# Performance work log

Measured on AMD Instinct MI355X. Metric: run time of the kernel, lower is better.

The kernel has to match this reference:

```python
import jax, jax.numpy as jnp
import numpy as np

B, T, E, A, S, H = 1024, 64, 1024, 10, 30, 200  # batch, time, embed, actdim, stoch, deter==hidden
MIN_STD = 0.1


def _xavier(key, fan_in, fan_out):
    lim = float(np.sqrt(6.0 / (fan_in + fan_out)))
    return jax.random.uniform(key, (fan_in, fan_out), jnp.float32, -lim, lim)


def setup_inputs() -> dict:
    key = jax.random.key(0)
    ks = jax.random.split(key, 20)
    gl = 1.0 / float(np.sqrt(H))  # torch GRUCell default init bound
    inp = {
        'embed': jax.random.normal(ks[0], (B, T, E), jnp.float32),
        'action': jax.random.normal(ks[1], (B, T, A), jnp.float32),
        'eps_post': jax.random.normal(ks[2], (T, B, S), jnp.float32),
        'eps_prior': jax.random.normal(ks[3], (T, B, S), jnp.float32),
        # Linear weights stored [in, out] (transposed vs torch) so x @ W works.
        'img1_w': _xavier(ks[4], A + S, H), 'img1_b': jnp.zeros((H,), jnp.float32),
        'gru_wi': jax.random.uniform(ks[5], (H, 3 * H), jnp.float32, -gl, gl),
        'gru_wh': jax.random.uniform(ks[6], (H, 3 * H), jnp.float32, -gl, gl),
        'gru_bi': jax.random.uniform(ks[7], (3 * H,), jnp.float32, -gl, gl),
        'gru_bh': jax.random.uniform(ks[8], (3 * H,), jnp.float32, -gl, gl),
        'img2_w': _xavier(ks[9], H, H), 'img2_b': jnp.zeros((H,), jnp.float32),
        'img3_w': _xavier(ks[10], H, 2 * S), 'img3_b': jnp.zeros((2 * S,), jnp.float32),
        'obs1_w': _xavier(ks[11], H + E, H), 'obs1_b': jnp.zeros((H,), jnp.float32),
        'obs2_w': _xavier(ks[12], H, 2 * S), 'obs2_b': jnp.zeros((2 * S,), jnp.float32),
    }
    return inp


def _observe(embed, action, eps_post, eps_prior,
             img1_w, img1_b, gru_wi, gru_wh, gru_bi, gru_bh,
             img2_w, img2_b, img3_w, img3_b, obs1_w, obs1_b, obs2_w, obs2_b):
    elu = jax.nn.elu
    embed_t = jnp.transpose(embed, (1, 0, 2))   # [T,B,E]
    action_t = jnp.transpose(action, (1, 0, 2))  # [T,B,A]

    def step(carry, xs):
        stoch, deter = carry
        a, emb, ep_q, ep_p = xs
        # img_step (prior)
        x = elu(jnp.concatenate([stoch, a], -1) @ img1_w + img1_b)
        gi = x @ gru_wi + gru_bi
        gh = deter @ gru_wh + gru_bh
        ir, iz, i_n = jnp.split(gi, 3, axis=-1)
        hr, hz, h_n = jnp.split(gh, 3, axis=-1)
        r = jax.nn.sigmoid(ir + hr)
        z = jax.nn.sigmoid(iz + hz)
        n = jnp.tanh(i_n + r * h_n)
        deter = (1.0 - z) * n + z * deter
        y = elu(deter @ img2_w + img2_b) @ img3_w + img3_b
        p_mean, p_std = jnp.split(y, 2, axis=-1)
        p_std = jax.nn.softplus(p_std) + MIN_STD
        p_stoch = p_mean + p_std * ep_p  # rsample
        # obs_step (posterior)
        o = elu(jnp.concatenate([deter, emb], -1) @ obs1_w + obs1_b) @ obs2_w + obs2_b
        q_mean, q_std = jnp.split(o, 2, axis=-1)
        q_std = jax.nn.softplus(q_std) + MIN_STD
        q_stoch = q_mean + q_std * ep_q  # rsample
        out = jnp.concatenate([q_mean, q_std, q_stoch, deter,
                               p_mean, p_std, p_stoch, deter], axis=-1)
        return (q_stoch, deter), out

    init = (jnp.zeros((B, S), embed.dtype), jnp.zeros((B, H), embed.dtype))
    _, outs = jax.lax.scan(step, init, (action_t, embed_t, eps_post, eps_prior))
    # outs: [T, B, 2*(3S+H)] -> [B, T, 580]; layout: post(mean,std,stoch,deter)|prior(mean,std,stoch,deter)
    return jnp.transpose(outs, (1, 0, 2))


def reference(embed, action, eps_post, eps_prior,
              img1_w, img1_b, gru_wi, gru_wh, gru_bi, gru_bh,
              img2_w, img2_b, img3_w, img3_b, obs1_w, obs1_b, obs2_w, obs2_b):
    return _observe(embed, action, eps_post, eps_prior,
                    img1_w, img1_b, gru_wi, gru_wh, gru_bi, gru_bh,
                    img2_w, img2_b, img3_w, img3_b, obs1_w, obs1_b, obs2_w, obs2_b)
```

## Files before the change

kernel.cpp:

```cpp
#include <hip/hip_runtime.h>

#define T_ 64

typedef __attribute__((ext_vector_type(4))) float f32x4;
typedef __attribute__((ext_vector_type(8))) short s16x8;

__device__ __forceinline__ unsigned short f2bf(float f) {
  unsigned u = __float_as_uint(f);
  u = (u + 0x7FFFu + ((u >> 16) & 1u)) >> 16;
  return (unsigned short)u;
}
__device__ __forceinline__ float bf2f(unsigned short h) {
  return __uint_as_float(((unsigned)h) << 16);
}
__device__ __forceinline__ float eluf(float x) { return x > 0.f ? x : __expf(x) - 1.f; }
__device__ __forceinline__ float sigmf(float x) { return 1.f / (1.f + __expf(-x)); }
__device__ __forceinline__ float tanh_(float x) {
  float xx = fminf(fmaxf(x, -30.f), 30.f);
  float e = __expf(-2.f * xx);
  return (1.f - e) / (1.f + e);
}
__device__ __forceinline__ float softpf(float x) {
  return x > 20.f ? x : __logf(1.f + __expf(x));
}

#define OPW1   0
#define OPWI   6656
#define OPWH   126464
#define OPO1D  246272
#define OPO2   286208
#define OPI2   298496
#define OPI3   345088
#define OWIWT  359424
#define OWHWT  364416
#define OO1DWT 369408
#define OI1WT  371072
#define OO2WT  372736
#define PK_U16 373248

#define OFF_PK  26214400
#define OFF_SWZ 26960896

__device__ void pack_mat(int idx, int stride, const float* __restrict__ W,
                         int K, int N, int KT, int NT, unsigned short* __restrict__ dst) {
  int total = KT * NT * 512;
  for (int i = idx; i < total; i += stride) {
    int j = i & 7, l = (i >> 3) & 63, rem = i >> 9;
    int kt = rem % KT, nt = rem / KT;
    int n = nt * 16 + (l & 15), k = kt * 32 + (l >> 4) * 8 + j;
    float v = (k < K && n < N) ? W[(size_t)k * N + n] : 0.f;
    dst[i] = f2bf(v);
  }
}

__device__ void pack_gate(int idx, int stride, const float* __restrict__ W,
                          unsigned short* __restrict__ dst) {
  int total = 3 * 13 * 6 * 512;
  for (int i = idx; i < total; i += stride) {
    int j = i & 7, l = (i >> 3) & 63, rem = i >> 9;
    int kt = rem % 6, rem2 = rem / 6, nt = rem2 % 13, g = rem2 / 13;
    int u = nt * 16 + (l & 15);
    int k = kt * 32 + (l >> 4) * 8 + j;
    float v = (u < 200) ? W[(size_t)k * 600 + g * 200 + u] : 0.f;
    dst[i] = f2bf(v);
  }
}

__global__ void prep_weights(const float* __restrict__ w1, const float* __restrict__ wi,
                             const float* __restrict__ wh, const float* __restrict__ i2,
                             const float* __restrict__ i3, const float* __restrict__ obs1w,
                             const float* __restrict__ o2,
                             unsigned short* __restrict__ pk,
                             unsigned short* __restrict__ swz) {
  int idx = blockIdx.x * blockDim.x + threadIdx.x;
  int stride = gridDim.x * blockDim.x;
  pack_mat(idx, stride, w1, 40, 200, 1, 13, pk + OPW1);
  pack_gate(idx, stride, wi, pk + OPWI);
  pack_gate(idx, stride, wh, pk + OPWH);
  pack_mat(idx, stride, obs1w, 200, 200, 6, 13, pk + OPO1D);
  pack_mat(idx, stride, o2, 200, 60, 6, 4, pk + OPO2);
  pack_mat(idx, stride, i2, 200, 200, 7, 13, pk + OPI2);
  pack_mat(idx, stride, i3, 200, 60, 7, 4, pk + OPI3);
  for (int i = idx; i < 4992; i += stride) {
    int j = i & 7, c = (i >> 3) % 208, g = i / 1664;
    pk[OWIWT + i] = f2bf((c < 200) ? wi[(size_t)(192 + j) * 600 + g * 200 + c] : 0.f);
    pk[OWHWT + i] = f2bf((c < 200) ? wh[(size_t)(192 + j) * 600 + g * 200 + c] : 0.f);
  }
  for (int i = idx; i < 1664; i += stride) {
    int c = i >> 3, j = i & 7;
    pk[OO1DWT + i] = f2bf((c < 200) ? obs1w[(size_t)(192 + j) * 200 + c] : 0.f);
    pk[OI1WT + i]  = f2bf((c < 200) ? w1[(size_t)(32 + j) * 200 + c] : 0.f);
  }
  for (int i = idx; i < 512; i += stride) {
    int c = i >> 3, j = i & 7;
    pk[OO2WT + i] = f2bf((c < 60) ? o2[(size_t)(192 + j) * 60 + c] : 0.f);
  }
  for (int i = idx; i < 212992; i += stride) {
    int j = i & 7, l = (i >> 3) & 63, rem = i >> 9;
    int nt = rem % 13, kc = rem / 13;
    int k = kc * 32 + ((l >> 4) * 8) + j;
    int n = nt * 16 + (l & 15);
    float v = (n < 200) ? obs1w[(size_t)(200 + k) * 200 + n] : 0.0f;
    swz[i] = f2bf(v);
  }
}

__global__ __launch_bounds__(256) void emb_gemm(const float* __restrict__ embed,
                                                const float* __restrict__ obs1b,
                                                const unsigned short* __restrict__ swz,
                                                unsigned short* __restrict__ emb_pre) {
  __shared__ __align__(16) unsigned short lds_A[64][40];
  int tid = threadIdx.x;
  int lane = tid & 63, w = tid >> 6;
  int R0 = blockIdx.x * 64;
  int tt = R0 >> 10;
  int bb = R0 & 1023;

  f32x4 acc[13];
#pragma unroll
  for (int nt = 0; nt < 13; ++nt) acc[nt] = (f32x4){0.f, 0.f, 0.f, 0.f};

  int i_row = tid >> 2, cg = tid & 3;
  const float* arow = embed + ((size_t)(bb + i_row) * 64 + tt) * 1024 + cg * 8;

  for (int kc = 0; kc < 32; ++kc) {
    __syncthreads();
    {
      const float* p = arow + kc * 32;
      f32x4 a0 = *(const f32x4*)p;
      f32x4 a1 = *(const f32x4*)(p + 4);
      unsigned short* dst = &lds_A[i_row][cg * 8];
      dst[0] = f2bf(a0[0]); dst[1] = f2bf(a0[1]); dst[2] = f2bf(a0[2]); dst[3] = f2bf(a0[3]);
      dst[4] = f2bf(a1[0]); dst[5] = f2bf(a1[1]); dst[6] = f2bf(a1[2]); dst[7] = f2bf(a1[3]);
    }
    __syncthreads();
    s16x8 af = *(const s16x8*)&lds_A[w * 16 + (lane & 15)][(lane >> 4) * 8];
    const unsigned short* bp = swz + (size_t)kc * 6656 + (size_t)lane * 8;
#pragma unroll
    for (int nt = 0; nt < 13; ++nt) {
      s16x8 bfv = *(const s16x8*)(bp + nt * 512);
      acc[nt] = __builtin_amdgcn_mfma_f32_16x16x32_bf16(af, bfv, acc[nt], 0, 0, 0);
    }
  }
  int r0 = R0 + w * 16 + ((lane >> 4) << 2);
  int c0 = lane & 15;
#pragma unroll
  for (int nt = 0; nt < 13; ++nt) {
    int n = nt * 16 + c0;
    if (n < 200) {
      float bv = obs1b[n];
#pragma unroll
      for (int rr = 0; rr < 4; ++rr)
        emb_pre[(size_t)(r0 + rr) * 200 + n] = f2bf(acc[nt][rr] + bv);
    }
  }
}

#define LGKM0  asm volatile("s_waitcnt lgkmcnt(0)" ::: "memory")
#define MEMCLB asm volatile("" ::: "memory")
#define BAR()  __builtin_amdgcn_s_barrier()
#define MFMA16(A, B, C) __builtin_amdgcn_mfma_f32_16x16x32_bf16((A), (B), (C), 0, 0, 0)
#define WV9  asm volatile("s_waitcnt vmcnt(9)" ::: "memory")
#define WV29 asm volatile("s_waitcnt vmcnt(29)" ::: "memory")
#define WV4  asm volatile("s_waitcnt vmcnt(4)" ::: "memory")
#define WV0  asm volatile("s_waitcnt vmcnt(0)" ::: "memory")

typedef __attribute__((address_space(3))) unsigned int u32_lds;
typedef const __attribute__((address_space(1))) unsigned int u32_glb;

__device__ __forceinline__ void gll16(const unsigned short* g, unsigned short* l, int lane) {
  __builtin_amdgcn_global_load_lds((u32_glb*)(g + lane * 8), (u32_lds*)l, 16, 0, 0);
}

template <int TB, bool BIGB>
__device__ __forceinline__ f32x4 cons6(const s16x8* A, f32x4 acc,
                                       unsigned short* ringw, const unsigned* toffw,
                                       const unsigned short* pk, int lane) {
#pragma unroll
  for (int kt = 0; kt < 6; ++kt) {
    const int tau = TB + kt;
    if ((tau & 3) == 0) {
      if (tau < 8) { if (BIGB) { WV29; } else { WV9; } }
      else { WV4; }
    }
    s16x8 Bv = *(const s16x8*)(ringw + (tau & 7) * 512 + lane * 8);
    acc = MFMA16(A[kt], Bv, acc);
    if ((tau & 3) == 3) {
      LGKM0; MEMCLB;
#pragma unroll
      for (int k2 = 1; k2 <= 4; ++k2) {
        const int tile = (tau + 4 + k2) % 48;
        gll16(pk + toffw[tile], ringw + (tile & 7) * 512, lane);
      }
      MEMCLB;
    }
  }
  return acc;
}

__device__ __forceinline__ f32x4 res6(const s16x8* A, const s16x8* Wt, f32x4 acc) {
#pragma unroll
  for (int kt = 0; kt < 6; ++kt) acc = MFMA16(A[kt], Wt[kt], acc);
  return acc;
}
__device__ __forceinline__ f32x4 rem1(const s16x8& A6, const unsigned short* wt,
                                      const unsigned short* zb, bool kg0, f32x4 acc) {
  const unsigned short* p = kg0 ? wt : zb;
  return MFMA16(A6, *(const s16x8*)p, acc);
}
__device__ __forceinline__ void grustep(const f32x4& rv, const f32x4& zv,
                                        const f32x4& inv, const f32x4& hnv, f32x4& dv) {
#pragma unroll
  for (int rr = 0; rr < 4; ++rr) {
    float r = sigmf(rv[rr]);
    float z = sigmf(zv[rr]);
    float n = tanh_(inv[rr] + r * hnv[rr]);
    dv[rr] = (1.f - z) * n + z * dv[rr];
  }
}

__global__ __launch_bounds__(512, 1) void scan_v7(
    const float* __restrict__ action, const float* __restrict__ eps_post,
    const float* __restrict__ img1_b, const float* __restrict__ gru_bi,
    const float* __restrict__ gru_bh, const float* __restrict__ obs2_b,
    const unsigned short* __restrict__ pk, const unsigned short* __restrict__ emb_pre,
    float* __restrict__ out) {

  __shared__ __align__(16) unsigned short ring[8][8][512];
  __shared__ __align__(16) unsigned short l_w1[13 * 512];
  __shared__ __align__(16) unsigned short l_wiWT[3][208][8];
  __shared__ __align__(16) unsigned short l_whWT[3][208][8];
  __shared__ __align__(16) unsigned short l_o1dWT[208][8];
  __shared__ __align__(16) unsigned short l_i1WT[208][8];
  __shared__ __align__(16) unsigned short l_o2WT[64][8];
  __shared__ __align__(16) unsigned short zblk[8];
  __shared__ __align__(16) unsigned short xoA[28][16][8];
  __shared__ __align__(16) unsigned short dA[28][16][8];
  __shared__ __align__(16) unsigned short sA[8][16][8];
  __shared__ __align__(16) float s_o[60][20];
  __shared__ __align__(16) float outbuf[16][292];
  __shared__ unsigned l_toff[8][48];

  const int tid = threadIdx.x, lane = tid & 63, w = tid >> 6;
  const int arow = lane & 15, kg = lane >> 4;
  const bool kg0 = (kg == 0);
  const int b0 = blockIdx.x * 16;
  unsigned short* ringw = &ring[w][0][0];
  const unsigned* toffw = &l_toff[w][0];

  for (int i = tid; i < 28 * 16 * 8; i += 512) { (&xoA[0][0][0])[i] = 0; (&dA[0][0][0])[i] = 0; }
  for (int i = tid; i < 8 * 16 * 8; i += 512) (&sA[0][0][0])[i] = 0;
  for (int i = tid; i < 13 * 512; i += 512) l_w1[i] = pk[OPW1 + i];
  for (int i = tid; i < 4992; i += 512) {
    (&l_wiWT[0][0][0])[i] = pk[OWIWT + i];
    (&l_whWT[0][0][0])[i] = pk[OWHWT + i];
  }
  for (int i = tid; i < 1664; i += 512) {
    (&l_o1dWT[0][0])[i] = pk[OO1DWT + i];
    (&l_i1WT[0][0])[i] = pk[OI1WT + i];
  }
  for (int i = tid; i < 512; i += 512) (&l_o2WT[0][0])[i] = pk[OO2WT + i];
  if (tid < 8) zblk[tid] = 0;
  for (int i = tid; i < 8 * 48; i += 512) {
    int ww = i / 48, tau = i % 48;
    unsigned off;
    if (ww < 5) {
      if (tau < 18) { int g = tau / 6, kt = tau % 6; off = OPWI + ((g * 13 + ww) * 6 + kt) * 512; }
      else {
        int t2 = tau - 18, ug = ww + 8;
        if (t2 < 6)       off = OPWI + ((0 * 13 + ug) * 6 + t2) * 512;
        else if (t2 < 12) off = OPWI + ((1 * 13 + ug) * 6 + (t2 - 6)) * 512;
        else if (t2 < 18) off = OPWH + ((1 * 13 + ug) * 6 + (t2 - 12)) * 512;
        else if (t2 < 24) off = OPWI + ((2 * 13 + ug) * 6 + (t2 - 18)) * 512;
        else              off = OPWH + ((2 * 13 + ug) * 6 + (t2 - 24)) * 512;
      }
    } else {
      if (tau < 18) { int g = tau / 6, kt = tau % 6; off = OPWI + ((g * 13 + ww) * 6 + kt) * 512; }
      else if (tau < 42) {
        int i4 = (tau - 18) / 6, kt = (tau - 18) % 6;
        int nt = (ww - 5) * 4 + i4;
        off = OPO1D + (nt * 6 + kt) * 512;
      } else {
        int kt = tau - 42;
        int nt5 = (ww == 5) ? 0 : (ww == 6) ? 1 : 3;
        off = OPO2 + (nt5 * 6 + kt) * 512;
      }
    }
    l_toff[ww][tau] = off;
  }

  s16x8 wB[4][6];
  {
    const unsigned short* base[4];
    if (w < 5) {
      base[0] = pk + OPWH + (size_t)((0 * 13 + w) * 6) * 512;
      base[1] = pk + OPWH + (size_t)((1 * 13 + w) * 6) * 512;
      base[2] = pk + OPWH + (size_t)((2 * 13 + w) * 6) * 512;
      base[3] = pk + OPWH + (size_t)((0 * 13 + w + 8) * 6) * 512;
    } else {
      base[0] = pk + OPWH + (size_t)((0 * 13 + w) * 6) * 512;
      base[1] = pk + OPWH + (size_t)((1 * 13 + w) * 6) * 512;
      base[2] = pk + OPWH + (size_t)((2 * 13 + w) * 6) * 512;
      if (w == 5)      base[3] = pk + OPO1D + (size_t)(12 * 6) * 512;
      else if (w == 7) base[3] = pk + OPO2 + (size_t)(2 * 6) * 512;
      else             base[3] = pk + OPO1D;
    }
#pragma unroll
    for (int s = 0; s < 4; ++s)
#pragma unroll
      for (int kt = 0; kt < 6; ++kt)
        wB[s][kt] = *(const s16x8*)(base[s] + (size_t)kt * 512 + lane * 8);
  }

  const int uA = w * 16 + arow;
  const int uB = (w + 8) * 16 + arow;
  const bool mB = (w < 5) && (uB < 200);
  const int uBc = (uB < 200) ? uB : 199;
  float bsA0 = gru_bi[uA] + gru_bh[uA];
  float bsA1 = gru_bi[200 + uA] + gru_bh[200 + uA];
  float bi2a = gru_bi[400 + uA], bh2a = gru_bh[400 + uA];
  float bsB0 = mB ? (gru_bi[uBc] + gru_bh[uBc]) : 0.f;
  float bsB1 = mB ? (gru_bi[200 + uBc] + gru_bh[200 + uBc]) : 0.f;
  float bi2b = mB ? gru_bi[400 + uBc] : 0.f;
  float bh2b = mB ? gru_bh[400 + uBc] : 0.f;
  float b1A = img1_b[uA];
  float b1B = mB ? img1_b[uBc] : 0.f;
  float b5a = 0.f, b5b = 0.f;
  if (w == 5) b5a = obs2_b[arow];
  else if (w == 6) b5a = obs2_b[16 + arow];
  else if (w == 7) { b5a = (48 + arow < 60) ? obs2_b[48 + arow] : 0.f; b5b = obs2_b[32 + arow]; }

  unsigned short e16[20];
#pragma unroll
  for (int i = 0; i < 20; ++i) e16[i] = 0;
  if (w >= 5) {
#pragma unroll
    for (int i = 0; i < 5; ++i) {
      int nt = (w == 5) ? ((i < 4) ? i : 12) : ((w == 6) ? (4 + ((i < 4) ? i : 3)) : (8 + ((i < 4) ? i : 3)));
      int c = nt * 16 + arow; int cc = (c < 200) ? c : 199;
#pragma unroll
      for (int rr = 0; rr < 4; ++rr)
        e16[i * 4 + rr] = emb_pre[((size_t)(b0 + kg * 4 + rr)) * 200 + cc];
    }
  }
  float epsv;
  { int it = (tid < 480) ? tid : 479;
    epsv = eps_post[((size_t)(b0 + it / 30)) * 30 + it % 30]; }
  float act0, actn;
  { int sl = (lane < 20) ? (w * 20 + lane) : (w * 20);
    act0 = action[((size_t)(b0 + sl / 10) * T_ + 0) * 10 + sl % 10];
    actn = action[((size_t)(b0 + sl / 10) * T_ + 1) * 10 + sl % 10]; }
  f32x4 dv0 = {0.f, 0.f, 0.f, 0.f}, dv1 = {0.f, 0.f, 0.f, 0.f};

  __syncthreads();
  if (lane < 20) {
    int sl = w * 20 + lane; int kk = sl % 10, r = sl / 10;
    sA[(30 + kk) >> 3][r][(30 + kk) & 7] = f2bf(act0);
  }
#pragma unroll
  for (int tt = 0; tt < 8; ++tt) gll16(pk + toffw[tt], ringw + tt * 512, lane);
  WV0;
  __syncthreads();

  for (int t = 0; t < T_; ++t) {
    {
      s16x8 a0 = *(const s16x8*)&sA[kg][arow][0];
      s16x8 a1 = *(const s16x8*)&sA[4 + kg][arow][0];
      {
        s16x8 B0 = *(const s16x8*)&l_w1[w * 512 + lane * 8];
        f32x4 acc = {b1A, b1A, b1A, b1A};
        acc = MFMA16(a0, B0, acc);
        acc = rem1(a1, &l_i1WT[uA][0], zblk, kg0, acc);
#pragma unroll
        for (int rr = 0; rr < 4; ++rr)
          xoA[uA >> 3][kg * 4 + rr][uA & 7] = f2bf(eluf(acc[rr]));
      }
      if (w < 5) {
        s16x8 B0 = *(const s16x8*)&l_w1[(w + 8) * 512 + lane * 8];
        f32x4 acc = {b1B, b1B, b1B, b1B};
        acc = MFMA16(a0, B0, acc);
        acc = rem1(a1, &l_i1WT[uB][0], zblk, kg0, acc);
        if (uB < 200) {
#pragma unroll
          for (int rr = 0; rr < 4; ++rr)
            xoA[uB >> 3][kg * 4 + rr][uB & 7] = f2bf(eluf(acc[rr]));
        }
      }
    }
    LGKM0; BAR();

    {
      s16x8 ax[6], ad[6];
#pragma unroll
      for (int kt = 0; kt < 6; ++kt) {
        ax[kt] = *(const s16x8*)&xoA[kt * 4 + kg][arow][0];
        ad[kt] = *(const s16x8*)&dA[kt * 4 + kg][arow][0];
      }
      s16x8 ax6 = *(const s16x8*)&xoA[24 + kg][arow][0];
      s16x8 ad6 = *(const s16x8*)&dA[24 + kg][arow][0];
      if (w < 5) {
        f32x4 rv = cons6<0, false>(ax, (f32x4){bsA0, bsA0, bsA0, bsA0}, ringw, toffw, pk, lane);
        rv = rem1(ax6, &l_wiWT[0][uA][0], zblk, kg0, rv);
        rv = res6(ad, wB[0], rv);
        rv = rem1(ad6, &l_whWT[0][uA][0], zblk, kg0, rv);
        f32x4 zv = cons6<6, false>(ax, (f32x4){bsA1, bsA1, bsA1, bsA1}, ringw, toffw, pk, lane);
        zv = rem1(ax6, &l_wiWT[1][uA][0], zblk, kg0, zv);
        zv = res6(ad, wB[1], zv);
        zv = rem1(ad6, &l_whWT[1][uA][0], zblk, kg0, zv);
        f32x4 inv = cons6<12, false>(ax, (f32x4){bi2a, bi2a, bi2a, bi2a}, ringw, toffw, pk, lane);
        inv = rem1(ax6, &l_wiWT[2][uA][0], zblk, kg0, inv);
        f32x4 hnv = res6(ad, wB[2], (f32x4){bh2a, bh2a, bh2a, bh2a});
        hnv = rem1(ad6, &l_whWT[2][uA][0], zblk, kg0, hnv);
        grustep(rv, zv, inv, hnv, dv0);
#pragma unroll
        for (int rr = 0; rr < 4; ++rr) outbuf[kg * 4 + rr][90 + uA] = dv0[rr];
        f32x4 rv2 = cons6<18, false>(ax, (f32x4){bsB0, bsB0, bsB0, bsB0}, ringw, toffw, pk, lane);
        rv2 = rem1(ax6, &l_wiWT[0][uB][0], zblk, kg0, rv2);
        rv2 = res6(ad, wB[3], rv2);
        rv2 = rem1(ad6, &l_whWT[0][uB][0], zblk, kg0, rv2);
        f32x4 zv2 = cons6<24, false>(ax, (f32x4){bsB1, bsB1, bsB1, bsB1}, ringw, toffw, pk, lane);
        zv2 = cons6<30, false>(ad, zv2, ringw, toffw, pk, lane);
        zv2 = rem1(ax6, &l_wiWT[1][uB][0], zblk, kg0, zv2);
        zv2 = rem1(ad6, &l_whWT[1][uB][0], zblk, kg0, zv2);
        f32x4 inv2 = cons6<36, false>(ax, (f32x4){bi2b, bi2b, bi2b, bi2b}, ringw, toffw, pk, lane);
        inv2 = rem1(ax6, &l_wiWT[2][uB][0], zblk, kg0, inv2);
        f32x4 hnv2 = cons6<42, false>(ad, (f32x4){bh2b, bh2b, bh2b, bh2b}, ringw, toffw, pk, lane);
        hnv2 = rem1(ad6, &l_whWT[2][uB][0], zblk, kg0, hnv2);
        grustep(rv2, zv2, inv2, hnv2, dv1);
        if (uB < 200) {
#pragma unroll
          for (int rr = 0; rr < 4; ++rr) outbuf[kg * 4 + rr][90 + uB] = dv1[rr];
        }
      } else {
        f32x4 rv = cons6<0, true>(ax, (f32x4){bsA0, bsA0, bsA0, bsA0}, ringw, toffw, pk, lane);
        rv = rem1(ax6, &l_wiWT[0][uA][0], zblk, kg0, rv);
        rv = res6(ad, wB[0], rv);
        rv = rem1(ad6, &l_whWT[0][uA][0], zblk, kg0, rv);
        f32x4 zv = cons6<6, true>(ax, (f32x4){bsA1, bsA1, bsA1, bsA1}, ringw, toffw, pk, lane);
        zv = rem1(ax6, &l_wiWT[1][uA][0], zblk, kg0, zv);
        zv = res6(ad, wB[1], zv);
        zv = rem1(ad6, &l_whWT[1][uA][0], zblk, kg0, zv);
        f32x4 inv = cons6<12, true>(ax, (f32x4){bi2a, bi2a, bi2a, bi2a}, ringw, toffw, pk, lane);
        inv = rem1(ax6, &l_wiWT[2][uA][0], zblk, kg0, inv);
        f32x4 hnv = res6(ad, wB[2], (f32x4){bh2a, bh2a, bh2a, bh2a});
        hnv = rem1(ad6, &l_whWT[2][uA][0], zblk, kg0, hnv);
        grustep(rv, zv, inv, hnv, dv0);
#pragma unroll
        for (int rr = 0; rr < 4; ++rr) outbuf[kg * 4 + rr][90 + uA] = dv0[rr];
      }
    }
    LGKM0; BAR();

    {
#pragma unroll
      for (int rr = 0; rr < 4; ++rr)
        dA[uA >> 3][kg * 4 + rr][uA & 7] = f2bf(dv0[rr]);
      if (mB) {
#pragma unroll
        for (int rr = 0; rr < 4; ++rr)
          dA[uB >> 3][kg * 4 + rr][uB & 7] = f2bf(dv1[rr]);
      }
    }
    LGKM0; BAR();

    if (w >= 5) {
      s16x8 ad4[6];
#pragma unroll
      for (int kt = 0; kt < 6; ++kt) ad4[kt] = *(const s16x8*)&dA[kt * 4 + kg][arow][0];
      s16x8 ad46 = *(const s16x8*)&dA[24 + kg][arow][0];
      const int ntb = (w - 5) * 4;
      {
        int c = (ntb + 0) * 16 + arow;
        f32x4 acc = cons6<18, true>(ad4, (f32x4){0.f, 0.f, 0.f, 0.f}, ringw, toffw, pk, lane);
        acc = rem1(ad46, &l_o1dWT[c][0], zblk, kg0, acc);
#pragma unroll
        for (int rr = 0; rr < 4; ++rr)
          xoA[c >> 3][kg * 4 + rr][c & 7] = f2bf(eluf(acc[rr] + bf2f(e16[0 * 4 + rr])));
      }
      {
        int c = (ntb + 1) * 16 + arow;
        f32x4 acc = cons6<24, true>(ad4, (f32x4){0.f, 0.f, 0.f, 0.f}, ringw, toffw, pk, lane);
        acc = rem1(ad46, &l_o1dWT[c][0], zblk, kg0, acc);
#pragma unroll
        for (int rr = 0; rr < 4; ++rr)
          xoA[c >> 3][kg * 4 + rr][c & 7] = f2bf(eluf(acc[rr] + bf2f(e16[1 * 4 + rr])));
      }
      {
        int c = (ntb + 2) * 16 + arow;
        f32x4 acc = cons6<30, true>(ad4, (f32x4){0.f, 0.f, 0.f, 0.f}, ringw, toffw, pk, lane);
        acc = rem1(ad46, &l_o1dWT[c][0], zblk, kg0, acc);
#pragma unroll
        for (int rr = 0; rr < 4; ++rr)
          xoA[c >> 3][kg * 4 + rr][c & 7] = f2bf(eluf(acc[rr] + bf2f(e16[2 * 4 + rr])));
      }
      {
        int c = (ntb + 3) * 16 + arow;
        f32x4 acc = cons6<36, true>(ad4, (f32x4){0.f, 0.f, 0.f, 0.f}, ringw, toffw, pk, lane);
        acc = rem1(ad46, &l_o1dWT[c][0], zblk, kg0, acc);
#pragma unroll
        for (int rr = 0; rr < 4; ++rr)
          xoA[c >> 3][kg * 4 + rr][c & 7] = f2bf(eluf(acc[rr] + bf2f(e16[3 * 4 + rr])));
      }
      if (w == 5) {
        int c = 192 + arow;
        f32x4 acc = res6(ad4, wB[3], (f32x4){0.f, 0.f, 0.f, 0.f});
        acc = rem1(ad46, &l_o1dWT[c][0], zblk, kg0, acc);
        if (c < 200) {
#pragma unroll
          for (int rr = 0; rr < 4; ++rr)
            xoA[c >> 3][kg * 4 + rr][c & 7] = f2bf(eluf(acc[rr] + bf2f(e16[16 + rr])));
        }
      }
    }
    LGKM0; BAR();

    if (w >= 5) {
      s16x8 a5[6];
#pragma unroll
      for (int kt = 0; kt < 6; ++kt) a5[kt] = *(const s16x8*)&xoA[kt * 4 + kg][arow][0];
      s16x8 a56 = *(const s16x8*)&xoA[24 + kg][arow][0];
      int c5 = (w == 5) ? arow : (w == 6) ? (16 + arow) : (48 + arow);
      f32x4 acc = cons6<42, true>(a5, (f32x4){b5a, b5a, b5a, b5a}, ringw, toffw, pk, lane);
      {
        int c5c = (c5 < 64) ? c5 : 63;
        acc = rem1(a56, &l_o2WT[c5c][0], zblk, kg0, acc);
      }
      if (c5 < 60) *(f32x4*)&s_o[c5][kg * 4] = acc;
      if (w == 7) {
        int c5r = 32 + arow;
        f32x4 acc2 = res6(a5, wB[3], (f32x4){b5b, b5b, b5b, b5b});
        acc2 = rem1(a56, &l_o2WT[c5r][0], zblk, kg0, acc2);
        *(f32x4*)&s_o[c5r][kg * 4] = acc2;
      }
    }
    LGKM0; BAR();

    MEMCLB;
    {
      if (tid < 480) {
        int r = tid / 30, j = tid % 30;
        float qm = s_o[j][r];
        float qs = softpf(s_o[j + 30][r]) + 0.1f;
        float qst = qm + qs * epsv;
        outbuf[r][j] = qm; outbuf[r][30 + j] = qs; outbuf[r][60 + j] = qst;
        sA[j >> 3][r][j & 7] = f2bf(qst);
      }
      if (lane < 20) {
        int sl = w * 20 + lane; int kk = sl % 10, r = sl / 10;
        sA[(30 + kk) >> 3][r][(30 + kk) & 7] = f2bf(actn);
      }
      int tc = (t + 1 < T_) ? t + 1 : T_ - 1;
      int ta = (t + 2 < T_) ? t + 2 : T_ - 1;
      MEMCLB;
      if (w >= 5) {
#pragma unroll
        for (int i = 0; i < 5; ++i) {
          int nt = (w == 5) ? ((i < 4) ? i : 12) : ((w == 6) ? (4 + ((i < 4) ? i : 3)) : (8 + ((i < 4) ? i : 3)));
          int c = nt * 16 + arow; int cc = (c < 200) ? c : 199;
#pragma unroll
          for (int rr = 0; rr < 4; ++rr)
            e16[i * 4 + rr] = emb_pre[((size_t)tc * 1024 + b0 + kg * 4 + rr) * 200 + cc];
        }
      }
      { int it = (tid < 480) ? tid : 479;
        epsv = eps_post[((size_t)tc * 1024 + b0 + it / 30) * 30 + it % 30]; }
      { int sl = (lane < 20) ? (w * 20 + lane) : (w * 20);
        actn = action[((size_t)(b0 + sl / 10) * T_ + ta) * 10 + sl % 10]; }
      MEMCLB;
    }
    LGKM0; BAR();

#pragma unroll
    for (int k2 = 0; k2 < 3; ++k2) {
      int idx = tid + k2 * 512; idx = (idx < 1168) ? idx : 1167;
      int row = idx / 73, ci = idx - row * 73;
      f32x4 v = *(const f32x4*)&outbuf[row][ci * 4];
      *(f32x4*)(out + ((size_t)(b0 + row) * T_ + t) * 580 + ci * 4) = v;
    }
    MEMCLB;
  }
}

__global__ __launch_bounds__(256) void post_head(const float* __restrict__ eps_prior,
                                                 const float* __restrict__ img2_b,
                                                 const float* __restrict__ img3_b,
                                                 const unsigned short* __restrict__ pk,
                                                 float* __restrict__ out) {
  __shared__ __align__(16) unsigned short dAp[4][28][16][8];
  __shared__ __align__(16) unsigned short y1p[4][28][16][8];
  __shared__ __align__(16) float s_p[60][68];
  int b = blockIdx.x;
  int tid = threadIdx.x;
  int lane = tid & 63, w = tid >> 6, arow = lane & 15, kg = lane >> 4;

  for (int i = tid; i < 1536; i += 256) {
    int mt = i / 384, rem = i % 384;
    int gidx = 25 + rem / 128, r2 = (rem % 128) / 8, j = rem & 7;
    dAp[mt][gidx][r2][j] = 0;
    y1p[mt][gidx][r2][j] = 0;
  }
  for (int i = tid; i < 12800; i += 256) {
    int row = i / 200, c = i % 200;
    float v = out[((size_t)(b * 64 + row)) * 580 + 90 + c];
    dAp[row >> 4][c >> 3][row & 15][c & 7] = f2bf(v);
  }
  __syncthreads();

  s16x8 ad[7];
#pragma unroll
  for (int kt = 0; kt < 7; ++kt) ad[kt] = *(const s16x8*)&dAp[w][kt * 4 + kg][arow][0];
#pragma unroll
  for (int nt = 0; nt < 13; ++nt) {
    int col = nt * 16 + arow;
    float bv = (col < 200) ? img2_b[col] : 0.f;
    f32x4 acc = {bv, bv, bv, bv};
#pragma unroll
    for (int kt = 0; kt < 7; ++kt) {
      s16x8 Bv = *(const s16x8*)(pk + OPI2 + (size_t)((nt * 7 + kt) * 512) + lane * 8);
      acc = __builtin_amdgcn_mfma_f32_16x16x32_bf16(ad[kt], Bv, acc, 0, 0, 0);
    }
    if (col < 200) {
#pragma unroll
      for (int rr = 0; rr < 4; ++rr)
        y1p[w][col >> 3][kg * 4 + rr][col & 7] = f2bf(eluf(acc[rr]));
    }
  }
  __syncthreads();

  s16x8 ay[7];
#pragma unroll
  for (int kt = 0; kt < 7; ++kt) ay[kt] = *(const s16x8*)&y1p[w][kt * 4 + kg][arow][0];
#pragma unroll
  for (int nt = 0; nt < 4; ++nt) {
    int col = nt * 16 + arow;
    float bv = (col < 60) ? img3_b[col] : 0.f;
    f32x4 acc = {bv, bv, bv, bv};
#pragma unroll
    for (int kt = 0; kt < 7; ++kt) {
      s16x8 Bv = *(const s16x8*)(pk + OPI3 + (size_t)((nt * 7 + kt) * 512) + lane * 8);
      acc = __builtin_amdgcn_mfma_f32_16x16x32_bf16(ay[kt], Bv, acc, 0, 0, 0);
    }
    if (col < 60) {
#pragma unroll
      for (int rr = 0; rr < 4; ++rr) s_p[col][w * 16 + kg * 4 + rr] = acc[rr];
    }
  }
  __syncthreads();

  for (int i = tid; i < 1920; i += 256) {
    int row = i / 30, j = i % 30;
    float pm = s_p[j][row];
    float ps = softpf(s_p[j + 30][row]) + 0.1f;
    float pst = pm + ps * eps_prior[((size_t)row * 1024 + b) * 30 + j];
    size_t ob = ((size_t)b * 64 + row) * 580;
    out[ob + 290 + j] = pm;
    out[ob + 320 + j] = ps;
    out[ob + 350 + j] = pst;
  }
  for (int i = tid; i < 6400; i += 256) {
    int row = i / 100, c2 = i % 100;
    size_t ob = ((size_t)b * 64 + row) * 580;
    *(float2*)&out[ob + 380 + c2 * 2] = *(const float2*)&out[ob + 90 + c2 * 2];
  }
}

extern "C" void kernel_launch(void* const* d_in, const int* in_sizes, int n_in,
                              void* d_out, int out_size, void* d_ws, size_t ws_size,
                              hipStream_t stream) {
  const float* embed    = (const float*)d_in[0];
  const float* action   = (const float*)d_in[1];
  const float* eps_post = (const float*)d_in[2];
  const float* eps_prior= (const float*)d_in[3];
  const float* img1_w   = (const float*)d_in[4];
  const float* img1_b   = (const float*)d_in[5];
  const float* gru_wi   = (const float*)d_in[6];
  const float* gru_wh   = (const float*)d_in[7];
  const float* gru_bi   = (const float*)d_in[8];
  const float* gru_bh   = (const float*)d_in[9];
  const float* img2_w   = (const float*)d_in[10];
  const float* img2_b   = (const float*)d_in[11];
  const float* img3_w   = (const float*)d_in[12];
  const float* img3_b   = (const float*)d_in[13];
  const float* obs1_w   = (const float*)d_in[14];
  const float* obs1_b   = (const float*)d_in[15];
  const float* obs2_w   = (const float*)d_in[16];
  const float* obs2_b   = (const float*)d_in[17];

  char* ws = (char*)d_ws;
  unsigned short* emb_pre = (unsigned short*)ws;
  unsigned short* pkw     = (unsigned short*)(ws + OFF_PK);
  unsigned short* swz     = (unsigned short*)(ws + OFF_SWZ);
  float* outp = (float*)d_out;

  prep_weights<<<256, 256, 0, stream>>>(img1_w, gru_wi, gru_wh, img2_w, img3_w,
                                        obs1_w, obs2_w, pkw, swz);
  emb_gemm<<<1024, 256, 0, stream>>>(embed, obs1_b, swz, emb_pre);
  scan_v7<<<64, 512, 0, stream>>>(action, eps_post, img1_b, gru_bi, gru_bh,
                                  obs2_b, pkw, emb_pre, outp);
  post_head<<<1024, 256, 0, stream>>>(eps_prior, img2_b, img3_b, pkw, outp);
}
```

Measured before the change: 1.067 ms.

## Replace LDS ring-buffer weight streaming with register triple-buffered global loads

The recurrent scan kernel stops streaming its per-step GRU and obs weight tiles through an LDS ring with global_load_lds and hand-placed vmcnt waits. Each wave now prefetches 6-tile groups straight into registers from global memory, rotating three buffers so the next group loads while the current one feeds MFMAs. Fewer weight groups stay resident in registers, the work split for the obs2 head moves between waves 6 and 7, and the explicit memory clobbers are removed. This drops the LDS ring and its waitcnt bookkeeping but raises register pressure, and latency hiding now depends on the compiler's scheduling. It also relaxes launch bounds and takes __restrict__ off pk.

```diff
diff --git a/kernel.cpp b/kernel.cpp
--- a/kernel.cpp
+++ b/kernel.cpp
@@ -157,47 +157,19 @@
 }
 
 #define LGKM0  asm volatile("s_waitcnt lgkmcnt(0)" ::: "memory")
-#define MEMCLB asm volatile("" ::: "memory")
 #define BAR()  __builtin_amdgcn_s_barrier()
 #define MFMA16(A, B, C) __builtin_amdgcn_mfma_f32_16x16x32_bf16((A), (B), (C), 0, 0, 0)
-#define WV9  asm volatile("s_waitcnt vmcnt(9)" ::: "memory")
-#define WV29 asm volatile("s_waitcnt vmcnt(29)" ::: "memory")
-#define WV4  asm volatile("s_waitcnt vmcnt(4)" ::: "memory")
-#define WV0  asm volatile("s_waitcnt vmcnt(0)" ::: "memory")
-
-typedef __attribute__((address_space(3))) unsigned int u32_lds;
-typedef const __attribute__((address_space(1))) unsigned int u32_glb;
-
-__device__ __forceinline__ void gll16(const unsigned short* g, unsigned short* l, int lane) {
-  __builtin_amdgcn_global_load_lds((u32_glb*)(g + lane * 8), (u32_lds*)l, 16, 0, 0);
-}
-
-template <int TB, bool BIGB>
-__device__ __forceinline__ f32x4 cons6(const s16x8* A, f32x4 acc,
-                                       unsigned short* ringw, const unsigned* toffw,
-                                       const unsigned short* pk, int lane) {
-#pragma unroll
-  for (int kt = 0; kt < 6; ++kt) {
-    const int tau = TB + kt;
-    if ((tau & 3) == 0) {
-      if (tau < 8) { if (BIGB) { WV29; } else { WV9; } }
-      else { WV4; }
-    }
-    s16x8 Bv = *(const s16x8*)(ringw + (tau & 7) * 512 + lane * 8);
-    acc = MFMA16(A[kt], Bv, acc);
-    if ((tau & 3) == 3) {
-      LGKM0; MEMCLB;
-#pragma unroll
-      for (int k2 = 1; k2 <= 4; ++k2) {
-        const int tile = (tau + 4 + k2) % 48;
-        gll16(pk + toffw[tile], ringw + (tile & 7) * 512, lane);
-      }
-      MEMCLB;
-    }
-  }
-  return acc;
-}
-
+
+__device__ __forceinline__ unsigned opq(unsigned x) {
+  asm volatile("" : "+v"(x));
+  return x;
+}
+__device__ __forceinline__ void ld6(const unsigned short* pk, unsigned off, int lane, s16x8* B) {
+  const unsigned short* p = pk + off + lane * 8;
+#pragma unroll
+  for (int kt = 0; kt < 6; ++kt)
+    B[kt] = *(const s16x8*)(p + kt * 512);
+}
 __device__ __forceinline__ f32x4 res6(const s16x8* A, const s16x8* Wt, f32x4 acc) {
 #pragma unroll
   for (int kt = 0; kt < 6; ++kt) acc = MFMA16(A[kt], Wt[kt], acc);
@@ -219,14 +191,13 @@
   }
 }
 
-__global__ __launch_bounds__(512, 1) void scan_v7(
+__global__ __launch_bounds__(512) void scan_v8(
     const float* __restrict__ action, const float* __restrict__ eps_post,
     const float* __restrict__ img1_b, const float* __restrict__ gru_bi,
     const float* __restrict__ gru_bh, const float* __restrict__ obs2_b,
-    const unsigned short* __restrict__ pk, const unsigned short* __restrict__ emb_pre,
+    const unsigned short* pk, const unsigned short* __restrict__ emb_pre,
     float* __restrict__ out) {
 
-  __shared__ __align__(16) unsigned short ring[8][8][512];
   __shared__ __align__(16) unsigned short l_w1[13 * 512];
   __shared__ __align__(16) unsigned short l_wiWT[3][208][8];
   __shared__ __align__(16) unsigned short l_whWT[3][208][8];
@@ -239,14 +210,11 @@
   __shared__ __align__(16) unsigned short sA[8][16][8];
   __shared__ __align__(16) float s_o[60][20];
   __shared__ __align__(16) float outbuf[16][292];
-  __shared__ unsigned l_toff[8][48];
 
   const int tid = threadIdx.x, lane = tid & 63, w = tid >> 6;
   const int arow = lane & 15, kg = lane >> 4;
   const bool kg0 = (kg == 0);
   const int b0 = blockIdx.x * 16;
-  unsigned short* ringw = &ring[w][0][0];
-  const unsigned* toffw = &l_toff[w][0];
 
   for (int i = tid; i < 28 * 16 * 8; i += 512) { (&xoA[0][0][0])[i] = 0; (&dA[0][0][0])[i] = 0; }
   for (int i = tid; i < 8 * 16 * 8; i += 512) (&sA[0][0][0])[i] = 0;
@@ -261,55 +229,40 @@
   }
   for (int i = tid; i < 512; i += 512) (&l_o2WT[0][0])[i] = pk[OO2WT + i];
   if (tid < 8) zblk[tid] = 0;
-  for (int i = tid; i < 8 * 48; i += 512) {
-    int ww = i / 48, tau = i % 48;
-    unsigned off;
-    if (ww < 5) {
-      if (tau < 18) { int g = tau / 6, kt = tau % 6; off = OPWI + ((g * 13 + ww) * 6 + kt) * 512; }
-      else {
-        int t2 = tau - 18, ug = ww + 8;
-        if (t2 < 6)       off = OPWI + ((0 * 13 + ug) * 6 + t2) * 512;
-        else if (t2 < 12) off = OPWI + ((1 * 13 + ug) * 6 + (t2 - 6)) * 512;
-        else if (t2 < 18) off = OPWH + ((1 * 13 + ug) * 6 + (t2 - 12)) * 512;
-        else if (t2 < 24) off = OPWI + ((2 * 13 + ug) * 6 + (t2 - 18)) * 512;
-        else              off = OPWH + ((2 * 13 + ug) * 6 + (t2 - 24)) * 512;
-      }
+
+  unsigned co[9];
+  {
+    if (w < 5) {
+      co[0] = OPWI + (unsigned)(((0 * 13 + w) * 6) * 512);
+      co[1] = OPWI + (unsigned)(((1 * 13 + w) * 6) * 512);
+      co[2] = OPWI + (unsigned)(((2 * 13 + w) * 6) * 512);
+      co[3] = OPWI + (unsigned)(((0 * 13 + w + 8) * 6) * 512);
+      co[4] = OPWH + (unsigned)(((0 * 13 + w + 8) * 6) * 512);
+      co[5] = OPWI + (unsigned)(((1 * 13 + w + 8) * 6) * 512);
+      co[6] = OPWH + (unsigned)(((1 * 13 + w + 8) * 6) * 512);
+      co[7] = OPWI + (unsigned)(((2 * 13 + w + 8) * 6) * 512);
+      co[8] = OPWH + (unsigned)(((2 * 13 + w + 8) * 6) * 512);
     } else {
-      if (tau < 18) { int g = tau / 6, kt = tau % 6; off = OPWI + ((g * 13 + ww) * 6 + kt) * 512; }
-      else if (tau < 42) {
-        int i4 = (tau - 18) / 6, kt = (tau - 18) % 6;
-        int nt = (ww - 5) * 4 + i4;
-        off = OPO1D + (nt * 6 + kt) * 512;
-      } else {
-        int kt = tau - 42;
-        int nt5 = (ww == 5) ? 0 : (ww == 6) ? 1 : 3;
-        off = OPO2 + (nt5 * 6 + kt) * 512;
-      }
-    }
-    l_toff[ww][tau] = off;
-  }
-
-  s16x8 wB[4][6];
-  {
-    const unsigned short* base[4];
-    if (w < 5) {
-      base[0] = pk + OPWH + (size_t)((0 * 13 + w) * 6) * 512;
-      base[1] = pk + OPWH + (size_t)((1 * 13 + w) * 6) * 512;
-      base[2] = pk + OPWH + (size_t)((2 * 13 + w) * 6) * 512;
-      base[3] = pk + OPWH + (size_t)((0 * 13 + w + 8) * 6) * 512;
-    } else {
-      base[0] = pk + OPWH + (size_t)((0 * 13 + w) * 6) * 512;
-      base[1] = pk + OPWH + (size_t)((1 * 13 + w) * 6) * 512;
-      base[2] = pk + OPWH + (size_t)((2 * 13 + w) * 6) * 512;
-      if (w == 5)      base[3] = pk + OPO1D + (size_t)(12 * 6) * 512;
-      else if (w == 7) base[3] = pk + OPO2 + (size_t)(2 * 6) * 512;
-      else             base[3] = pk + OPO1D;
-    }
-#pragma unroll
-    for (int s = 0; s < 4; ++s)
-#pragma unroll
-      for (int kt = 0; kt < 6; ++kt)
-        wB[s][kt] = *(const s16x8*)(base[s] + (size_t)kt * 512 + lane * 8);
+      co[0] = OPWI + (unsigned)(((0 * 13 + w) * 6) * 512);
+      co[1] = OPWI + (unsigned)(((1 * 13 + w) * 6) * 512);
+      co[2] = OPWI + (unsigned)(((2 * 13 + w) * 6) * 512);
+      int ntb = (w - 5) * 4;
+#pragma unroll
+      for (int i = 0; i < 4; ++i) co[3 + i] = OPO1D + (unsigned)(((ntb + i) * 6) * 512);
+      if (w == 5)      { co[7] = OPO1D + (unsigned)((12 * 6) * 512); co[8] = OPO2; }
+      else if (w == 6) { co[7] = OPO2 + (unsigned)((1 * 6) * 512); co[8] = OPO2 + (unsigned)((2 * 6) * 512); }
+      else             { co[7] = OPO2 + (unsigned)((3 * 6) * 512); co[8] = OPO2 + (unsigned)((3 * 6) * 512); }
+    }
+#pragma unroll
+    for (int c = 0; c < 9; ++c) co[c] = __builtin_amdgcn_readfirstlane(co[c]);
+  }
+
+  s16x8 wB0[6], wB1[6], wB2[6];
+#pragma unroll
+  for (int kt = 0; kt < 6; ++kt) {
+    wB0[kt] = *(const s16x8*)(pk + OPWH + (size_t)(((0 * 13 + w) * 6 + kt) * 512) + lane * 8);
+    wB1[kt] = *(const s16x8*)(pk + OPWH + (size_t)(((1 * 13 + w) * 6 + kt) * 512) + lane * 8);
+    wB2[kt] = *(const s16x8*)(pk + OPWH + (size_t)(((2 * 13 + w) * 6 + kt) * 512) + lane * 8);
   }
 
   const int uA = w * 16 + arow;
@@ -327,8 +280,8 @@
   float b1B = mB ? img1_b[uBc] : 0.f;
   float b5a = 0.f, b5b = 0.f;
   if (w == 5) b5a = obs2_b[arow];
-  else if (w == 6) b5a = obs2_b[16 + arow];
-  else if (w == 7) { b5a = (48 + arow < 60) ? obs2_b[48 + arow] : 0.f; b5b = obs2_b[32 + arow]; }
+  else if (w == 6) { b5a = obs2_b[16 + arow]; b5b = obs2_b[32 + arow]; }
+  else if (w == 7) b5a = (48 + arow < 60) ? obs2_b[48 + arow] : 0.f;
 
   unsigned short e16[20];
 #pragma unroll
@@ -336,11 +289,13 @@
   if (w >= 5) {
 #pragma unroll
     for (int i = 0; i < 5; ++i) {
-      int nt = (w == 5) ? ((i < 4) ? i : 12) : ((w == 6) ? (4 + ((i < 4) ? i : 3)) : (8 + ((i < 4) ? i : 3)));
-      int c = nt * 16 + arow; int cc = (c < 200) ? c : 199;
-#pragma unroll
-      for (int rr = 0; rr < 4; ++rr)
-        e16[i * 4 + rr] = emb_pre[((size_t)(b0 + kg * 4 + rr)) * 200 + cc];
+      if (i < 4 || w == 5) {
+        int nt = (i < 4) ? ((w - 5) * 4 + i) : 12;
+        int c = nt * 16 + arow; int cc = (c < 200) ? c : 199;
+#pragma unroll
+        for (int rr = 0; rr < 4; ++rr)
+          e16[i * 4 + rr] = emb_pre[((size_t)(b0 + kg * 4 + rr)) * 200 + cc];
+      }
     }
   }
   float epsv;
@@ -357,10 +312,10 @@
     int sl = w * 20 + lane; int kk = sl % 10, r = sl / 10;
     sA[(30 + kk) >> 3][r][(30 + kk) & 7] = f2bf(act0);
   }
-#pragma unroll
-  for (int tt = 0; tt < 8; ++tt) gll16(pk + toffw[tt], ringw + tt * 512, lane);
-  WV0;
-  __syncthreads();
+  s16x8 Bu0[6], Bu1[6], Bu2[6];
+  ld6(pk, opq(co[0]), lane, Bu0);
+  ld6(pk, opq(co[1]), lane, Bu1);
+  LGKM0; BAR();
 
   for (int t = 0; t < T_; ++t) {
     {
@@ -379,7 +334,7 @@
         s16x8 B0 = *(const s16x8*)&l_w1[(w + 8) * 512 + lane * 8];
         f32x4 acc = {b1B, b1B, b1B, b1B};
         acc = MFMA16(a0, B0, acc);
-        acc = rem1(a1, &l_i1WT[uB][0], zblk, kg0, acc);
+        acc = rem1(a1, &l_i1WT[uBc][0], zblk, kg0, acc);
         if (uB < 200) {
 #pragma unroll
           for (int rr = 0; rr < 4; ++rr)
@@ -399,50 +354,74 @@
       s16x8 ax6 = *(const s16x8*)&xoA[24 + kg][arow][0];
       s16x8 ad6 = *(const s16x8*)&dA[24 + kg][arow][0];
       if (w < 5) {
-        f32x4 rv = cons6<0, false>(ax, (f32x4){bsA0, bsA0, bsA0, bsA0}, ringw, toffw, pk, lane);
+        ld6(pk, opq(co[2]), lane, Bu2);
+        f32x4 rv = {bsA0, bsA0, bsA0, bsA0};
+        rv = res6(ax, Bu0, rv);
         rv = rem1(ax6, &l_wiWT[0][uA][0], zblk, kg0, rv);
-        rv = res6(ad, wB[0], rv);
+        rv = res6(ad, wB0, rv);
         rv = rem1(ad6, &l_whWT[0][uA][0], zblk, kg0, rv);
-        f32x4 zv = cons6<6, false>(ax, (f32x4){bsA1, bsA1, bsA1, bsA1}, ringw, toffw, pk, lane);
+        ld6(pk, opq(co[3]), lane, Bu0);
+        f32x4 zv = {bsA1, bsA1, bsA1, bsA1};
+        zv = res6(ax, Bu1, zv);
         zv = rem1(ax6, &l_wiWT[1][uA][0], zblk, kg0, zv);
-        zv = res6(ad, wB[1], zv);
+        zv = res6(ad, wB1, zv);
         zv = rem1(ad6, &l_whWT[1][uA][0], zblk, kg0, zv);
-        f32x4 inv = cons6<12, false>(ax, (f32x4){bi2a, bi2a, bi2a, bi2a}, ringw, toffw, pk, lane);
+        ld6(pk, opq(co[4]), lane, Bu1);
+        f32x4 inv = {bi2a, bi2a, bi2a, bi2a};
+        inv = res6(ax, Bu2, inv);
         inv = rem1(ax6, &l_wiWT[2][uA][0], zblk, kg0, inv);
-        f32x4 hnv = res6(ad, wB[2], (f32x4){bh2a, bh2a, bh2a, bh2a});
+        f32x4 hnv = {bh2a, bh2a, bh2a, bh2a};
+        hnv = res6(ad, wB2, hnv);
         hnv = rem1(ad6, &l_whWT[2][uA][0], zblk, kg0, hnv);
         grustep(rv, zv, inv, hnv, dv0);
 #pragma unroll
         for (int rr = 0; rr < 4; ++rr) outbuf[kg * 4 + rr][90 + uA] = dv0[rr];
-        f32x4 rv2 = cons6<18, false>(ax, (f32x4){bsB0, bsB0, bsB0, bsB0}, ringw, toffw, pk, lane);
-        rv2 = rem1(ax6, &l_wiWT[0][uB][0], zblk, kg0, rv2);
-        rv2 = res6(ad, wB[3], rv2);
-        rv2 = rem1(ad6, &l_whWT[0][uB][0], zblk, kg0, rv2);
-        f32x4 zv2 = cons6<24, false>(ax, (f32x4){bsB1, bsB1, bsB1, bsB1}, ringw, toffw, pk, lane);
-        zv2 = cons6<30, false>(ad, zv2, ringw, toffw, pk, lane);
-        zv2 = rem1(ax6, &l_wiWT[1][uB][0], zblk, kg0, zv2);
-        zv2 = rem1(ad6, &l_whWT[1][uB][0], zblk, kg0, zv2);
-        f32x4 inv2 = cons6<36, false>(ax, (f32x4){bi2b, bi2b, bi2b, bi2b}, ringw, toffw, pk, lane);
-        inv2 = rem1(ax6, &l_wiWT[2][uB][0], zblk, kg0, inv2);
-        f32x4 hnv2 = cons6<42, false>(ad, (f32x4){bh2b, bh2b, bh2b, bh2b}, ringw, toffw, pk, lane);
-        hnv2 = rem1(ad6, &l_whWT[2][uB][0], zblk, kg0, hnv2);
+        ld6(pk, opq(co[5]), lane, Bu2);
+        f32x4 rv2 = {bsB0, bsB0, bsB0, bsB0};
+        rv2 = res6(ax, Bu0, rv2);
+        rv2 = rem1(ax6, &l_wiWT[0][uBc][0], zblk, kg0, rv2);
+        ld6(pk, opq(co[6]), lane, Bu0);
+        rv2 = res6(ad, Bu1, rv2);
+        rv2 = rem1(ad6, &l_whWT[0][uBc][0], zblk, kg0, rv2);
+        ld6(pk, opq(co[7]), lane, Bu1);
+        f32x4 zv2 = {bsB1, bsB1, bsB1, bsB1};
+        zv2 = res6(ax, Bu2, zv2);
+        zv2 = rem1(ax6, &l_wiWT[1][uBc][0], zblk, kg0, zv2);
+        ld6(pk, opq(co[8]), lane, Bu2);
+        zv2 = res6(ad, Bu0, zv2);
+        zv2 = rem1(ad6, &l_whWT[1][uBc][0], zblk, kg0, zv2);
+        ld6(pk, opq(co[0]), lane, Bu0);
+        f32x4 inv2 = {bi2b, bi2b, bi2b, bi2b};
+        inv2 = res6(ax, Bu1, inv2);
+        inv2 = rem1(ax6, &l_wiWT[2][uBc][0], zblk, kg0, inv2);
+        ld6(pk, opq(co[1]), lane, Bu1);
+        f32x4 hnv2 = {bh2b, bh2b, bh2b, bh2b};
+        hnv2 = res6(ad, Bu2, hnv2);
+        hnv2 = rem1(ad6, &l_whWT[2][uBc][0], zblk, kg0, hnv2);
         grustep(rv2, zv2, inv2, hnv2, dv1);
         if (uB < 200) {
 #pragma unroll
           for (int rr = 0; rr < 4; ++rr) outbuf[kg * 4 + rr][90 + uB] = dv1[rr];
         }
       } else {
-        f32x4 rv = cons6<0, true>(ax, (f32x4){bsA0, bsA0, bsA0, bsA0}, ringw, toffw, pk, lane);
+        ld6(pk, opq(co[2]), lane, Bu2);
+        f32x4 rv = {bsA0, bsA0, bsA0, bsA0};
+        rv = res6(ax, Bu0, rv);
         rv = rem1(ax6, &l_wiWT[0][uA][0], zblk, kg0, rv);
-        rv = res6(ad, wB[0], rv);
+        rv = res6(ad, wB0, rv);
         rv = rem1(ad6, &l_whWT[0][uA][0], zblk, kg0, rv);
-        f32x4 zv = cons6<6, true>(ax, (f32x4){bsA1, bsA1, bsA1, bsA1}, ringw, toffw, pk, lane);
+        ld6(pk, opq(co[3]), lane, Bu0);
+        f32x4 zv = {bsA1, bsA1, bsA1, bsA1};
+        zv = res6(ax, Bu1, zv);
         zv = rem1(ax6, &l_wiWT[1][uA][0], zblk, kg0, zv);
-        zv = res6(ad, wB[1], zv);
+        zv = res6(ad, wB1, zv);
         zv = rem1(ad6, &l_whWT[1][uA][0], zblk, kg0, zv);
-        f32x4 inv = cons6<12, true>(ax, (f32x4){bi2a, bi2a, bi2a, bi2a}, ringw, toffw, pk, lane);
+        ld6(pk, opq(co[4]), lane, Bu1);
+        f32x4 inv = {bi2a, bi2a, bi2a, bi2a};
+        inv = res6(ax, Bu2, inv);
         inv = rem1(ax6, &l_wiWT[2][uA][0], zblk, kg0, inv);
-        f32x4 hnv = res6(ad, wB[2], (f32x4){bh2a, bh2a, bh2a, bh2a});
+        f32x4 hnv = {bh2a, bh2a, bh2a, bh2a};
+        hnv = res6(ad, wB2, hnv);
         hnv = rem1(ad6, &l_whWT[2][uA][0], zblk, kg0, hnv);
         grustep(rv, zv, inv, hnv, dv0);
 #pragma unroll
@@ -471,39 +450,44 @@
       const int ntb = (w - 5) * 4;
       {
         int c = (ntb + 0) * 16 + arow;
-        f32x4 acc = cons6<18, true>(ad4, (f32x4){0.f, 0.f, 0.f, 0.f}, ringw, toffw, pk, lane);
+        ld6(pk, opq(co[5]), lane, Bu2);
+        f32x4 acc = res6(ad4, Bu0, (f32x4){0.f, 0.f, 0.f, 0.f});
         acc = rem1(ad46, &l_o1dWT[c][0], zblk, kg0, acc);
 #pragma unroll
         for (int rr = 0; rr < 4; ++rr)
-          xoA[c >> 3][kg * 4 + rr][c & 7] = f2bf(eluf(acc[rr] + bf2f(e16[0 * 4 + rr])));
+          xoA[c >> 3][kg * 4 + rr][c & 7] = f2bf(eluf(acc[rr] + bf2f(e16[0 + rr])));
       }
       {
         int c = (ntb + 1) * 16 + arow;
-        f32x4 acc = cons6<24, true>(ad4, (f32x4){0.f, 0.f, 0.f, 0.f}, ringw, toffw, pk, lane);
+        ld6(pk, opq(co[6]), lane, Bu0);
+        f32x4 acc = res6(ad4, Bu1, (f32x4){0.f, 0.f, 0.f, 0.f});
         acc = rem1(ad46, &l_o1dWT[c][0], zblk, kg0, acc);
 #pragma unroll
         for (int rr = 0; rr < 4; ++rr)
-          xoA[c >> 3][kg * 4 + rr][c & 7] = f2bf(eluf(acc[rr] + bf2f(e16[1 * 4 + rr])));
+          xoA[c >> 3][kg * 4 + rr][c & 7] = f2bf(eluf(acc[rr] + bf2f(e16[4 + rr])));
       }
       {
         int c = (ntb + 2) * 16 + arow;
-        f32x4 acc = cons6<30, true>(ad4, (f32x4){0.f, 0.f, 0.f, 0.f}, ringw, toffw, pk, lane);
+        ld6(pk, opq(co[7]), lane, Bu1);
+        f32x4 acc = res6(ad4, Bu2, (f32x4){0.f, 0.f, 0.f, 0.f});
         acc = rem1(ad46, &l_o1dWT[c][0], zblk, kg0, acc);
 #pragma unroll
         for (int rr = 0; rr < 4; ++rr)
-          xoA[c >> 3][kg * 4 + rr][c & 7] = f2bf(eluf(acc[rr] + bf2f(e16[2 * 4 + rr])));
+          xoA[c >> 3][kg * 4 + rr][c & 7] = f2bf(eluf(acc[rr] + bf2f(e16[8 + rr])));
       }
       {
         int c = (ntb + 3) * 16 + arow;
-        f32x4 acc = cons6<36, true>(ad4, (f32x4){0.f, 0.f, 0.f, 0.f}, ringw, toffw, pk, lane);
+        ld6(pk, opq(co[8]), lane, Bu2);
+        f32x4 acc = res6(ad4, Bu0, (f32x4){0.f, 0.f, 0.f, 0.f});
         acc = rem1(ad46, &l_o1dWT[c][0], zblk, kg0, acc);
 #pragma unroll
         for (int rr = 0; rr < 4; ++rr)
-          xoA[c >> 3][kg * 4 + rr][c & 7] = f2bf(eluf(acc[rr] + bf2f(e16[3 * 4 + rr])));
+          xoA[c >> 3][kg * 4 + rr][c & 7] = f2bf(eluf(acc[rr] + bf2f(e16[12 + rr])));
       }
       if (w == 5) {
         int c = 192 + arow;
-        f32x4 acc = res6(ad4, wB[3], (f32x4){0.f, 0.f, 0.f, 0.f});
+        ld6(pk, opq(co[0]), lane, Bu0);
+        f32x4 acc = res6(ad4, Bu1, (f32x4){0.f, 0.f, 0.f, 0.f});
         acc = rem1(ad46, &l_o1dWT[c][0], zblk, kg0, acc);
         if (c < 200) {
 #pragma unroll
@@ -519,23 +503,32 @@
 #pragma unroll
       for (int kt = 0; kt < 6; ++kt) a5[kt] = *(const s16x8*)&xoA[kt * 4 + kg][arow][0];
       s16x8 a56 = *(const s16x8*)&xoA[24 + kg][arow][0];
-      int c5 = (w == 5) ? arow : (w == 6) ? (16 + arow) : (48 + arow);
-      f32x4 acc = cons6<42, true>(a5, (f32x4){b5a, b5a, b5a, b5a}, ringw, toffw, pk, lane);
-      {
+      if (w == 5) {
+        ld6(pk, opq(co[1]), lane, Bu1);
+        f32x4 acc = res6(a5, Bu2, (f32x4){b5a, b5a, b5a, b5a});
+        acc = rem1(a56, &l_o2WT[arow][0], zblk, kg0, acc);
+        *(f32x4*)&s_o[arow][kg * 4] = acc;
+      } else if (w == 6) {
+        ld6(pk, opq(co[0]), lane, Bu0);
+        f32x4 acc = res6(a5, Bu1, (f32x4){b5a, b5a, b5a, b5a});
+        acc = rem1(a56, &l_o2WT[16 + arow][0], zblk, kg0, acc);
+        *(f32x4*)&s_o[16 + arow][kg * 4] = acc;
+        ld6(pk, opq(co[1]), lane, Bu1);
+        f32x4 acc2 = res6(a5, Bu2, (f32x4){b5b, b5b, b5b, b5b});
+        acc2 = rem1(a56, &l_o2WT[32 + arow][0], zblk, kg0, acc2);
+        *(f32x4*)&s_o[32 + arow][kg * 4] = acc2;
+      } else {
+        ld6(pk, opq(co[0]), lane, Bu0);
+        int c5 = 48 + arow;
+        f32x4 acc = res6(a5, Bu1, (f32x4){b5a, b5a, b5a, b5a});
         int c5c = (c5 < 64) ? c5 : 63;
         acc = rem1(a56, &l_o2WT[c5c][0], zblk, kg0, acc);
-      }
-      if (c5 < 60) *(f32x4*)&s_o[c5][kg * 4] = acc;
-      if (w == 7) {
-        int c5r = 32 + arow;
-        f32x4 acc2 = res6(a5, wB[3], (f32x4){b5b, b5b, b5b, b5b});
-        acc2 = rem1(a56, &l_o2WT[c5r][0], zblk, kg0, acc2);
-        *(f32x4*)&s_o[c5r][kg * 4] = acc2;
+        if (c5 < 60) *(f32x4*)&s_o[c5][kg * 4] = acc;
+        ld6(pk, opq(co[1]), lane, Bu1);
       }
     }
     LGKM0; BAR();
 
-    MEMCLB;
     {
       if (tid < 480) {
         int r = tid / 30, j = tid % 30;
@@ -551,22 +544,22 @@
       }
       int tc = (t + 1 < T_) ? t + 1 : T_ - 1;
       int ta = (t + 2 < T_) ? t + 2 : T_ - 1;
-      MEMCLB;
       if (w >= 5) {
 #pragma unroll
         for (int i = 0; i < 5; ++i) {
-          int nt = (w == 5) ? ((i < 4) ? i : 12) : ((w == 6) ? (4 + ((i < 4) ? i : 3)) : (8 + ((i < 4) ? i : 3)));
-          int c = nt * 16 + arow; int cc = (c < 200) ? c : 199;
-#pragma unroll
-          for (int rr = 0; rr < 4; ++rr)
-            e16[i * 4 + rr] = emb_pre[((size_t)tc * 1024 + b0 + kg * 4 + rr) * 200 + cc];
+          if (i < 4 || w == 5) {
+            int nt = (i < 4) ? ((w - 5) * 4 + i) : 12;
+            int c = nt * 16 + arow; int cc = (c < 200) ? c : 199;
+#pragma unroll
+            for (int rr = 0; rr < 4; ++rr)
+              e16[i * 4 + rr] = emb_pre[((size_t)tc * 1024 + b0 + kg * 4 + rr) * 200 + cc];
+          }
         }
       }
       { int it = (tid < 480) ? tid : 479;
         epsv = eps_post[((size_t)tc * 1024 + b0 + it / 30) * 30 + it % 30]; }
       { int sl = (lane < 20) ? (w * 20 + lane) : (w * 20);
         actn = action[((size_t)(b0 + sl / 10) * T_ + ta) * 10 + sl % 10]; }
-      MEMCLB;
     }
     LGKM0; BAR();
 
@@ -577,7 +570,6 @@
       f32x4 v = *(const f32x4*)&outbuf[row][ci * 4];
       *(f32x4*)(out + ((size_t)(b0 + row) * T_ + t) * 580 + ci * 4) = v;
     }
-    MEMCLB;
   }
 }
 
@@ -695,7 +687,7 @@
   prep_weights<<<256, 256, 0, stream>>>(img1_w, gru_wi, gru_wh, img2_w, img3_w,
                                         obs1_w, obs2_w, pkw, swz);
   emb_gemm<<<1024, 256, 0, stream>>>(embed, obs1_b, swz, emb_pre);
-  scan_v7<<<64, 512, 0, stream>>>(action, eps_post, img1_b, gru_bi, gru_bh,
+  scan_v8<<<64, 512, 0, stream>>>(action, eps_post, img1_b, gru_bi, gru_bh,
                                   obs2_b, pkw, emb_pre, outp);
   post_head<<<1024, 256, 0, stream>>>(eps_prior, img2_b, img3_b, pkw, outp);
 }
```

New measurement: 1.105 ms. 3.6% more time.
